# Optimization experiments

Measured on AMD Instinct MI355X. Metric: run time of the kernel, lower is better.

## Reference

```python
import jax, jax.numpy as jnp
import numpy as np

B, T, C = 256, 512, 256
K = 8  # number of distinct phoneme classes used (indices into phoneme_inventory)
# weights dict {'aa':2.0,'ae':0.5,'ah':1.5,'ao':1.2,'aw':0.8}, rest default 1.0,
# materialized as a dense per-class-index weight vector:
WEIGHTS = np.ones(K, dtype=np.float32)
WEIGHTS[:5] = [2.0, 0.5, 1.5, 1.2, 0.8]


def setup_inputs() -> dict:
    key = jax.random.key(0)
    k1, k2 = jax.random.split(key)
    embeddings = jax.random.normal(k1, (B, T, C), dtype=jnp.float32)
    phonemes = jax.random.randint(k2, (B, T), 0, K, dtype=jnp.int64)
    weights = jnp.asarray(WEIGHTS)
    return {"embeddings": embeddings, "phonemes": phonemes, "weights": weights}


def reference(embeddings, phonemes, weights):
    Bs, Ts, Cs = embeddings.shape
    # F.normalize(p=2, dim=-1) with eps=1e-12
    norm = jnp.linalg.norm(embeddings, axis=-1, keepdims=True)
    emb = embeddings / jnp.maximum(norm, 1e-12)
    # all-pairs cosine similarity per timestep: [T, B, B]
    exp_sim = jnp.exp(jnp.einsum('itc,jtc->tij', emb, emb))
    eye = jnp.eye(Bs, dtype=bool)  # [B, B]
    p = phonemes.T  # [T, B]
    pos = (p[:, :, None] == p[:, None, :]) & ~eye  # [T, B, B]
    num = jnp.where(pos, exp_sim, 0.0).sum(-1)          # [T, B]
    den = jnp.where(~eye, exp_sim, 0.0).sum(-1)          # [T, B]
    per_sample = -jnp.log(num / (den + 1e-6))            # [T, B]
    # segment-mean per (timestep, class), then weighted mean over present classes
    oh = jax.nn.one_hot(p, weights.shape[0], dtype=per_sample.dtype)  # [T, B, K]
    counts = oh.sum(1)                                   # [T, K]
    sums = jnp.einsum('tb,tbk->tk', per_sample, oh)      # [T, K]
    present = counts > 0
    class_mean = sums / jnp.maximum(counts, 1.0)
    loss_t = jnp.where(present, class_mean * weights, 0.0).sum(-1) / present.sum(-1)
    return loss_t.mean()
```

## Files before the change

### kernel.cpp

```cpp
#include <hip/hip_runtime.h>

#define Bn 256
#define Tn 512
#define Cn 256
#define Kn 8

typedef __attribute__((ext_vector_type(4))) float f32x4;

__global__ __launch_bounds__(1024, 4)
void tcon_k(const float* __restrict__ emb,
            const int* __restrict__ phon,
            const float* __restrict__ wts,
            float* __restrict__ out) {
    __shared__ __align__(16) unsigned char Esh[2][Bn * Bn];
    __shared__ float invn[Bn];
    __shared__ int   pcls[2][Bn];
    __shared__ float num_s[2][Bn], den_s[2][Bn];
    __shared__ float csum[Kn];
    __shared__ int   ccnt[Kn];

    const int t0   = blockIdx.x * 2;
    const int t1   = t0 + 1;
    const int tid  = threadIdx.x;
    const int lane = tid & 63;
    const int wave = tid >> 6;
    const int rg   = wave >> 1;
    const int sh   = wave & 1;
    const int i0   = rg * 32;
    const int sd   = rg >> 1;
    const bool own = ((rg >> 2) == sh);
    const int fs   = own ? sd : (sh << 1);
    const int os   = own ? (sd ^ 1) : ((sh << 1) | 1);

    const int q   = lane >> 4;
    const int l15 = lane & 15;
    const int e3  = l15 & 7;

    if (tid < Kn) { csum[tid] = 0.0f; ccnt[tid] = 0; }
    if (tid < Bn) {
        pcls[0][tid] = phon[tid * Tn + t0];
        pcls[1][tid] = phon[tid * Tn + t1];
    }

    #pragma unroll 4
    for (int it = 0; it < 8; ++it) {
        const int f   = tid + it * 1024;
        const int row = f >> 5;
        const int b   = f & 31;
        const float4* p = (const float4*)(emb + ((size_t)row * Tn + t0) * Cn);
        const float4 v0 = p[2 * b];
        const float4 v1 = p[2 * b + 1];
        int lo = __builtin_amdgcn_cvt_pk_fp8_f32(v0.x, v0.y, 0, false);
        lo     = __builtin_amdgcn_cvt_pk_fp8_f32(v0.z, v0.w, lo, true);
        int hi = __builtin_amdgcn_cvt_pk_fp8_f32(v1.x, v1.y, 0, false);
        hi     = __builtin_amdgcn_cvt_pk_fp8_f32(v1.z, v1.w, hi, true);
        const int qq = b & 3, kk = b >> 2, kp = kk >> 1;
        const int ad = row * 256 + ((((qq << 2) + kp) ^ (row & 7)) << 4)
                     + ((kk & 1) << 3);
        int2 pk; pk.x = lo; pk.y = hi;
        *(int2*)&Esh[0][ad] = pk;
    }
    __syncthreads();

    f32x4 acc[2][4];

#define ZERO_ACC() do {                                                      \
    _Pragma("unroll") for (int _m = 0; _m < 2; ++_m)                         \
    _Pragma("unroll") for (int _n = 0; _n < 4; ++_n)                         \
        acc[_m][_n] = (f32x4){0.f, 0.f, 0.f, 0.f};                           \
} while (0)

#define STAGE4(ITBASE) do {                                                  \
    _Pragma("unroll") for (int _it = (ITBASE); _it < (ITBASE) + 4; ++_it) {  \
        const int _f   = tid + _it * 1024;                                   \
        const int _row = _f >> 5;                                            \
        const int _b   = _f & 31;                                            \
        const float4* _p = (const float4*)(emb + ((size_t)_row * Tn + t1) * Cn); \
        const float4 _v0 = _p[2 * _b];                                       \
        const float4 _v1 = _p[2 * _b + 1];                                   \
        int _lo = __builtin_amdgcn_cvt_pk_fp8_f32(_v0.x, _v0.y, 0, false);   \
        _lo     = __builtin_amdgcn_cvt_pk_fp8_f32(_v0.z, _v0.w, _lo, true);  \
        int _hi = __builtin_amdgcn_cvt_pk_fp8_f32(_v1.x, _v1.y, 0, false);   \
        _hi     = __builtin_amdgcn_cvt_pk_fp8_f32(_v1.z, _v1.w, _hi, true);  \
        const int _qq = _b & 3, _kk = _b >> 2, _kp = _kk >> 1;               \
        const int _ad = _row * 256 + ((((_qq << 2) + _kp) ^ (_row & 7)) << 4)\
                      + ((_kk & 1) << 3);                                    \
        int2 _pk; _pk.x = _lo; _pk.y = _hi;                                  \
        *(int2*)&Esh[1][_ad] = _pk;                                          \
    }                                                                        \
} while (0)

#define COMPUTE_STRIP(JB) do {                                               \
    ZERO_ACC();                                                              \
    _Pragma("unroll") for (int kp = 0; kp < 4; ++kp) {                       \
        const int sw = (((q << 2) + kp) ^ e3) << 4;                          \
        ulonglong2 _a[2], _b[4];                                             \
        _Pragma("unroll") for (int _m = 0; _m < 2; ++_m)                     \
            _a[_m] = *(const ulonglong2*)&Esh[tt][(i0 + _m * 16 + l15) * 256 + sw]; \
        _Pragma("unroll") for (int _n = 0; _n < 4; ++_n)                     \
            _b[_n] = *(const ulonglong2*)&Esh[tt][((JB) + _n * 16 + l15) * 256 + sw]; \
        _Pragma("unroll") for (int _m = 0; _m < 2; ++_m)                     \
        _Pragma("unroll") for (int _n = 0; _n < 4; ++_n) {                   \
            acc[_m][_n] = __builtin_amdgcn_mfma_f32_16x16x32_fp8_fp8(        \
                (long)_a[_m].x, (long)_b[_n].x, acc[_m][_n], 0, 0, 0);       \
            acc[_m][_n] = __builtin_amdgcn_mfma_f32_16x16x32_fp8_fp8(        \
                (long)_a[_m].y, (long)_b[_n].y, acc[_m][_n], 0, 0, 0);       \
        }                                                                    \
    }                                                                        \
} while (0)

#define EPILOGUE(JB) do {                                                    \
    _Pragma("unroll") for (int _n = 0; _n < 4; ++_n) {                       \
        const int _j  = (JB) + _n * 16 + l15;                                \
        const int _pj = pcls[tt][_j];                                        \
        const float _ij = invn[_j];                                          \
        _Pragma("unroll") for (int _m = 0; _m < 2; ++_m)                     \
        _Pragma("unroll") for (int _r = 0; _r < 4; ++_r) {                   \
            const int _e = _m * 4 + _r;                                      \
            const int _ir = i0 + _m * 16 + q * 4 + _r;                       \
            const float _ex = __expf(acc[_m][_n][_r] * inv_i[_e] * _ij);     \
            const bool _nd = (_ir != _j);                                    \
            den_p[_e] += _nd ? _ex : 0.0f;                                   \
            num_p[_e] += (_nd && (_pj == pi[_e])) ? _ex : 0.0f;              \
        }                                                                    \
    }                                                                        \
} while (0)

    #pragma unroll
    for (int tt = 0; tt < 2; ++tt) {
        COMPUTE_STRIP(fs * 64);
        if (own) {
            if ((rg & 1) == 0) {
                #pragma unroll
                for (int r = 0; r < 4; ++r)
                    if (l15 == q * 4 + r) {
                        invn[i0 + l15]      = rsqrtf(fmaxf(acc[0][0][r], 1e-24f));
                        invn[i0 + 16 + l15] = rsqrtf(fmaxf(acc[1][1][r], 1e-24f));
                    }
            } else {
                #pragma unroll
                for (int r = 0; r < 4; ++r)
                    if (l15 == q * 4 + r) {
                        invn[i0 + l15]      = rsqrtf(fmaxf(acc[0][2][r], 1e-24f));
                        invn[i0 + 16 + l15] = rsqrtf(fmaxf(acc[1][3][r], 1e-24f));
                    }
            }
        }
        if (tt == 0) STAGE4(0);
        __syncthreads();

        float num_p[8], den_p[8], inv_i[8];
        int   pi[8];
        #pragma unroll
        for (int e = 0; e < 8; ++e) {
            const int irow = i0 + (e >> 2) * 16 + q * 4 + (e & 3);
            num_p[e] = 0.0f; den_p[e] = 0.0f;
            pi[e]    = pcls[tt][irow];
            inv_i[e] = invn[irow];
        }

        EPILOGUE(fs * 64);
        if (tt == 0) STAGE4(4);
        COMPUTE_STRIP(os * 64);
        EPILOGUE(os * 64);

        #pragma unroll
        for (int e = 0; e < 8; ++e) {
            float n = num_p[e], d = den_p[e];
            #pragma unroll
            for (int m = 1; m <= 8; m <<= 1) {
                n += __shfl_xor(n, m, 64);
                d += __shfl_xor(d, m, 64);
            }
            if (l15 == e) {
                const int irow = i0 + (e >> 2) * 16 + q * 4 + (e & 3);
                num_s[sh][irow] = n;
                den_s[sh][irow] = d;
            }
        }
        __syncthreads();

        if (tid < Bn) {
            const float nn = num_s[0][tid] + num_s[1][tid];
            const float dd = den_s[0][tid] + den_s[1][tid];
            const float ps = __logf(dd + 1e-6f) - __logf(nn);
            const int c = pcls[tt][tid];
            atomicAdd(&csum[c], ps);
            atomicAdd(&ccnt[c], 1);
        }
        __syncthreads();

        if (tid == 0) {
            float accv = 0.0f; int np = 0;
            #pragma unroll
            for (int k = 0; k < Kn; ++k) {
                if (ccnt[k] > 0) { accv += (csum[k] / (float)ccnt[k]) * wts[k]; ++np; }
                csum[k] = 0.0f; ccnt[k] = 0;
            }
            atomicAdd(out, (accv / (float)np) * (1.0f / (float)Tn));
        }
    }
#undef ZERO_ACC
#undef STAGE4
#undef COMPUTE_STRIP
#undef EPILOGUE
}

extern "C" void kernel_launch(void* const* d_in, const int* in_sizes, int n_in,
                              void* d_out, int out_size, void* d_ws, size_t ws_size,
                              hipStream_t stream) {
    const float* emb  = (const float*)d_in[0];
    const int*   phon = (const int*)d_in[1];
    const float* wts  = (const float*)d_in[2];
    float*       out  = (float*)d_out;

    hipMemsetAsync(out, 0, sizeof(float), stream);
    tcon_k<<<Tn / 2, 1024, 0, stream>>>(emb, phon, wts, out);
}
```

Baseline: 226.6 us.

## Halve block to 512 threads with each wave covering all four column strips

The block shrinks from 1024 to 512 threads (8 waves). Each wave now owns 32 rows and loops over all four 64-column strips, so the split of columns across two half-waves and the two-slot num/den reduction go away. Staging of the second timestep's embeddings is spread over three points between strips, and sched_barriers keep that staging code in place. Each wave does more serial MFMA and epilogue work in exchange for fewer cross-wave partial sums, with occupancy hints set to 2 waves per EU.

```diff
diff --git a/kernel.cpp b/kernel.cpp
--- a/kernel.cpp
+++ b/kernel.cpp
@@ -7,7 +7,8 @@
 
 typedef __attribute__((ext_vector_type(4))) float f32x4;
 
-__global__ __launch_bounds__(1024, 4)
+__global__ __launch_bounds__(512)
+__attribute__((amdgpu_waves_per_eu(2, 2)))
 void tcon_k(const float* __restrict__ emb,
             const int* __restrict__ phon,
             const float* __restrict__ wts,
@@ -15,7 +16,7 @@
     __shared__ __align__(16) unsigned char Esh[2][Bn * Bn];
     __shared__ float invn[Bn];
     __shared__ int   pcls[2][Bn];
-    __shared__ float num_s[2][Bn], den_s[2][Bn];
+    __shared__ float num_s[Bn], den_s[Bn];
     __shared__ float csum[Kn];
     __shared__ int   ccnt[Kn];
 
@@ -24,13 +25,8 @@
     const int tid  = threadIdx.x;
     const int lane = tid & 63;
     const int wave = tid >> 6;
-    const int rg   = wave >> 1;
-    const int sh   = wave & 1;
-    const int i0   = rg * 32;
-    const int sd   = rg >> 1;
-    const bool own = ((rg >> 2) == sh);
-    const int fs   = own ? sd : (sh << 1);
-    const int os   = own ? (sd ^ 1) : ((sh << 1) | 1);
+    const int i0   = wave * 32;
+    const int sd   = wave >> 1;
 
     const int q   = lane >> 4;
     const int l15 = lane & 15;
@@ -43,8 +39,8 @@
     }
 
     #pragma unroll 4
-    for (int it = 0; it < 8; ++it) {
-        const int f   = tid + it * 1024;
+    for (int it = 0; it < 16; ++it) {
+        const int f   = tid + it * 512;
         const int row = f >> 5;
         const int b   = f & 31;
         const float4* p = (const float4*)(emb + ((size_t)row * Tn + t0) * Cn);
@@ -71,8 +67,9 @@
 } while (0)
 
 #define STAGE4(ITBASE) do {                                                  \
+    __builtin_amdgcn_sched_barrier(0);                                       \
     _Pragma("unroll") for (int _it = (ITBASE); _it < (ITBASE) + 4; ++_it) {  \
-        const int _f   = tid + _it * 1024;                                   \
+        const int _f   = tid + _it * 512;                                    \
         const int _row = _f >> 5;                                            \
         const int _b   = _f & 31;                                            \
         const float4* _p = (const float4*)(emb + ((size_t)_row * Tn + t1) * Cn); \
@@ -88,6 +85,7 @@
         int2 _pk; _pk.x = _lo; _pk.y = _hi;                                  \
         *(int2*)&Esh[1][_ad] = _pk;                                          \
     }                                                                        \
+    __builtin_amdgcn_sched_barrier(0);                                       \
 } while (0)
 
 #define COMPUTE_STRIP(JB) do {                                               \
@@ -128,23 +126,21 @@
 
     #pragma unroll
     for (int tt = 0; tt < 2; ++tt) {
-        COMPUTE_STRIP(fs * 64);
-        if (own) {
-            if ((rg & 1) == 0) {
-                #pragma unroll
-                for (int r = 0; r < 4; ++r)
-                    if (l15 == q * 4 + r) {
-                        invn[i0 + l15]      = rsqrtf(fmaxf(acc[0][0][r], 1e-24f));
-                        invn[i0 + 16 + l15] = rsqrtf(fmaxf(acc[1][1][r], 1e-24f));
-                    }
-            } else {
-                #pragma unroll
-                for (int r = 0; r < 4; ++r)
-                    if (l15 == q * 4 + r) {
-                        invn[i0 + l15]      = rsqrtf(fmaxf(acc[0][2][r], 1e-24f));
-                        invn[i0 + 16 + l15] = rsqrtf(fmaxf(acc[1][3][r], 1e-24f));
-                    }
-            }
+        COMPUTE_STRIP(sd * 64);
+        if ((wave & 1) == 0) {
+            #pragma unroll
+            for (int r = 0; r < 4; ++r)
+                if (l15 == q * 4 + r) {
+                    invn[i0 + l15]      = rsqrtf(fmaxf(acc[0][0][r], 1e-24f));
+                    invn[i0 + 16 + l15] = rsqrtf(fmaxf(acc[1][1][r], 1e-24f));
+                }
+        } else {
+            #pragma unroll
+            for (int r = 0; r < 4; ++r)
+                if (l15 == q * 4 + r) {
+                    invn[i0 + l15]      = rsqrtf(fmaxf(acc[0][2][r], 1e-24f));
+                    invn[i0 + 16 + l15] = rsqrtf(fmaxf(acc[1][3][r], 1e-24f));
+                }
         }
         if (tt == 0) STAGE4(0);
         __syncthreads();
@@ -159,10 +155,16 @@
             inv_i[e] = invn[irow];
         }
 
-        EPILOGUE(fs * 64);
+        EPILOGUE(sd * 64);
         if (tt == 0) STAGE4(4);
-        COMPUTE_STRIP(os * 64);
-        EPILOGUE(os * 64);
+        COMPUTE_STRIP((sd ^ 1) * 64);
+        EPILOGUE((sd ^ 1) * 64);
+        if (tt == 0) STAGE4(8);
+        COMPUTE_STRIP((sd ^ 2) * 64);
+        EPILOGUE((sd ^ 2) * 64);
+        if (tt == 0) STAGE4(12);
+        COMPUTE_STRIP((sd ^ 3) * 64);
+        EPILOGUE((sd ^ 3) * 64);
 
         #pragma unroll
         for (int e = 0; e < 8; ++e) {
@@ -174,16 +176,14 @@
             }
             if (l15 == e) {
                 const int irow = i0 + (e >> 2) * 16 + q * 4 + (e & 3);
-                num_s[sh][irow] = n;
-                den_s[sh][irow] = d;
+                num_s[irow] = n;
+                den_s[irow] = d;
             }
         }
         __syncthreads();
 
         if (tid < Bn) {
-            const float nn = num_s[0][tid] + num_s[1][tid];
-            const float dd = den_s[0][tid] + den_s[1][tid];
-            const float ps = __logf(dd + 1e-6f) - __logf(nn);
+            const float ps = __logf(den_s[tid] + 1e-6f) - __logf(num_s[tid]);
             const int c = pcls[tt][tid];
             atomicAdd(&csum[c], ps);
             atomicAdd(&ccnt[c], 1);
@@ -215,5 +215,5 @@
     float*       out  = (float*)d_out;
 
     hipMemsetAsync(out, 0, sizeof(float), stream);
-    tcon_k<<<Tn / 2, 1024, 0, stream>>>(emb, phon, wts, out);
+    tcon_k<<<Tn / 2, 512, 0, stream>>>(emb, phon, wts, out);
 }
```

New measurement: 217.6 us. 1.04x faster.
